# Optimization experiments

Measured on AMD Instinct MI355X. Metric: run time of the kernel, lower is better.

The kernel has to match this reference:

```python
import jax, jax.numpy as jnp
import numpy as np

MARGIN = 1.0
EPS = 1e-05
B = 8192
D = 128
NUM_CLASSES = 256


def setup_inputs() -> dict:
    key = jax.random.key(0)
    k1, k2 = jax.random.split(key)
    feature = jax.random.normal(k1, (B, D), dtype=jnp.float32)
    label = jax.random.randint(k2, (B,), 0, NUM_CLASSES, dtype=jnp.int32)
    return {"feature": feature, "label": label}


def reference(feature, label):
    # Pairwise Euclidean distance matrix: ||x_i||^2 + ||x_j||^2 - 2 x_i.x_j + eps, then sqrt
    sq = jnp.sum(feature * feature, axis=1, keepdims=True)  # [B, 1]
    dist = jnp.sqrt(jnp.maximum(sq + sq.T - 2.0 * (feature @ feature.T) + EPS, 0.0))  # [B, B]

    same = label[:, None] == label[None, :]  # [B, B] bool, includes self on diagonal
    inf = jnp.array(jnp.inf, dtype=dist.dtype)

    # Original sorts each row and takes same[1]: the SECOND smallest same-label distance
    # (the smallest is the anchor itself, distance sqrt(eps)).
    d_same = jnp.where(same, dist, inf)
    two_smallest = -jax.lax.top_k(-d_same, 2)[0]  # [B, 2], ascending smallest two
    pos = two_smallest[:, 1]  # nearest positive excluding self

    # diff.min(): hardest (closest) negative per row
    neg = jnp.min(jnp.where(same, inf, dist), axis=1)

    hinge = jnp.maximum(MARGIN + pos - neg, 0.0)
    return jnp.mean(hinge)
```

## Files before the change

kernel.cpp:

```cpp
#include <hip/hip_runtime.h>
#include <math.h>


#define BN 8192
#define MARGIN_F 1.0f
#define EPS_F 1e-5f

typedef __attribute__((ext_vector_type(8))) short short8;
typedef __attribute__((ext_vector_type(4))) float floatx4;

__device__ __forceinline__ unsigned short bf16_rne(float x, float& r) {
    unsigned u = __float_as_uint(x);
    u += 0x7FFF + ((u >> 16) & 1);
    unsigned short h = (unsigned short)(u >> 16);
    r = __uint_as_float(((unsigned)h) << 16);
    return h;
}

__global__ __launch_bounds__(256) void prep_kernel(const float* __restrict__ f,
                                                   const int* __restrict__ lbl,
                                                   short8* __restrict__ fbT,
                                                   float2* __restrict__ lsq,
                                                   float* __restrict__ g_acc,
                                                   unsigned* __restrict__ counter) {
    int gid = blockIdx.x * 256 + threadIdx.x;
    if (gid == 0) { *g_acc = 0.f; *counter = 0u; }
    int row = gid >> 3, part = gid & 7;
    const float4* f4 = (const float4*)f + (size_t)row * 32 + part * 4;
    float s = 0.f;
#pragma unroll
    for (int cc = 0; cc < 2; ++cc) {
        float4 v0 = f4[cc * 2], v1 = f4[cc * 2 + 1];
        float r0, r1, r2, r3, r4, r5, r6, r7;
        short8 o;
        o[0] = (short)bf16_rne(v0.x, r0);
        o[1] = (short)bf16_rne(v0.y, r1);
        o[2] = (short)bf16_rne(v0.z, r2);
        o[3] = (short)bf16_rne(v0.w, r3);
        o[4] = (short)bf16_rne(v1.x, r4);
        o[5] = (short)bf16_rne(v1.y, r5);
        o[6] = (short)bf16_rne(v1.z, r6);
        o[7] = (short)bf16_rne(v1.w, r7);
        fbT[(size_t)(part * 2 + cc) * BN + row] = o;
        s += r0 * r0 + r1 * r1 + r2 * r2 + r3 * r3 +
             r4 * r4 + r5 * r5 + r6 * r6 + r7 * r7;
    }
    s += __shfl_xor(s, 1, 8);
    s += __shfl_xor(s, 2, 8);
    s += __shfl_xor(s, 4, 8);
    if (part == 0) {
        float2 p;
        p.x = s;
        p.y = __int_as_float(lbl[row]);
        lsq[row] = p;
    }
}

__device__ __forceinline__ void stage_tile(const short8* __restrict__ fbT,
                                           short8* tile, int j0, int wv, int lane) {
#pragma unroll
    for (int it = 0; it < 2; ++it) {
        int s = wv * 128 + it * 64;
        int kc = (s >> 5) + (lane >> 5);
        int col = lane & 31;
        const short8* g = fbT + ((size_t)kc * BN + j0 + col);
        __builtin_amdgcn_global_load_lds(
            (const __attribute__((address_space(1))) void*)g,
            (__attribute__((address_space(3))) void*)(tile + s),
            16, 0, 0);
    }
}

__global__ __launch_bounds__(256, 2) void work_kernel(const short8* __restrict__ fbT,
                                                      const float2* __restrict__ lsq,
                                                      float* __restrict__ part_n1,
                                                      float* __restrict__ part_s1,
                                                      float* __restrict__ part_s2) {
    const int t = threadIdx.x;
    const int lane = t & 63;
    const int wv = t >> 6;
    const int q = lane >> 4, c = lane & 15;
    const int bid = blockIdx.x;

    __shared__ short8 Bt[2][512];
    __shared__ float2 lsq_sh[512];

    const int i0 = (bid & 31) * 256 + wv * 64;
    const int g = bid >> 5;
    const int jb = g * 512;

    stage_tile(fbT, Bt[0], jb, wv, lane);

    lsq_sh[t] = lsq[jb + t];
    lsq_sh[t + 256] = lsq[jb + t + 256];

    short8 a[4][4];
#pragma unroll
    for (int mf = 0; mf < 4; ++mf) {
        int row = i0 + mf * 16 + c;
#pragma unroll
        for (int ks = 0; ks < 4; ++ks)
            a[mf][ks] = fbT[(size_t)(ks * 4 + q) * BN + row];
    }
    int li[4][4];
#pragma unroll
    for (int mf = 0; mf < 4; ++mf)
#pragma unroll
        for (int rg = 0; rg < 4; ++rg)
            li[mf][rg] = __float_as_int(lsq[i0 + mf * 16 + q * 4 + rg].y);

#pragma unroll
    for (int mf = 0; mf < 4; ++mf) {
#pragma unroll
        for (int ks = 0; ks < 4; ++ks)
            asm volatile("" : "+v"(a[mf][ks]));
#pragma unroll
        for (int rg = 0; rg < 4; ++rg)
            asm volatile("" : "+v"(li[mf][rg]));
    }

    float n1[4][4], s1[4][4], s2[4][4];
#pragma unroll
    for (int mf = 0; mf < 4; ++mf)
#pragma unroll
        for (int rg = 0; rg < 4; ++rg) {
            n1[mf][rg] = INFINITY;
            s1[mf][rg] = INFINITY;
            s2[mf][rg] = INFINITY;
        }

    __syncthreads();

    for (int jt = 0; jt < 16; ++jt) {
        const short8* cur = Bt[jt & 1];
        const int j0 = jb + jt * 32;
        if (jt < 15) stage_tile(fbT, Bt[1 - (jt & 1)], j0 + 32, wv, lane);

        int ljv[2]; float sjv[2];
#pragma unroll
        for (int nf = 0; nf < 2; ++nf) {
            float2 p = lsq_sh[jt * 32 + nf * 16 + c];
            sjv[nf] = p.x;
            ljv[nf] = __float_as_int(p.y);
        }

        floatx4 acc[4][2];
#pragma unroll
        for (int mf = 0; mf < 4; ++mf)
#pragma unroll
            for (int nf = 0; nf < 2; ++nf) acc[mf][nf] = (floatx4)0.f;

#pragma unroll
        for (int ks = 0; ks < 4; ++ks) {
            short8 b[2];
#pragma unroll
            for (int nf = 0; nf < 2; ++nf)
                b[nf] = cur[(ks * 4 + q) * 32 + nf * 16 + c];
#pragma unroll
            for (int mf = 0; mf < 4; ++mf)
#pragma unroll
                for (int nf = 0; nf < 2; ++nf)
                    acc[mf][nf] = __builtin_amdgcn_mfma_f32_16x16x32_bf16(
                        a[mf][ks], b[nf], acc[mf][nf], 0, 0, 0);
        }

#pragma unroll
        for (int nf = 0; nf < 2; ++nf) {
#pragma unroll
            for (int mf = 0; mf < 4; ++mf)
#pragma unroll
                for (int rg = 0; rg < 4; ++rg) {
                    float v = fmaf(-2.0f, acc[mf][nf][rg], sjv[nf]);
                    bool same = (li[mf][rg] == ljv[nf]);
                    float vd = same ? INFINITY : v;
                    float vs = same ? v : INFINITY;
                    n1[mf][rg] = fminf(n1[mf][rg], vd);
                    s2[mf][rg] = fminf(s2[mf][rg], fmaxf(s1[mf][rg], vs));
                    s1[mf][rg] = fminf(s1[mf][rg], vs);
                }
        }
        __syncthreads();
    }

#pragma unroll
    for (int m = 1; m < 16; m <<= 1) {
#pragma unroll
        for (int mf = 0; mf < 4; ++mf)
#pragma unroll
            for (int rg = 0; rg < 4; ++rg) {
                n1[mf][rg] = fminf(n1[mf][rg], __shfl_xor(n1[mf][rg], m, 16));
                float o1 = __shfl_xor(s1[mf][rg], m, 16);
                float o2 = __shfl_xor(s2[mf][rg], m, 16);
                float hi = fminf(fmaxf(s1[mf][rg], o1), fminf(s2[mf][rg], o2));
                s1[mf][rg] = fminf(s1[mf][rg], o1);
                s2[mf][rg] = hi;
            }
    }
    if (c == 0) {
#pragma unroll
        for (int mf = 0; mf < 4; ++mf)
#pragma unroll
            for (int rg = 0; rg < 4; ++rg) {
                int idx = g * BN + i0 + mf * 16 + q * 4 + rg;
                part_n1[idx] = n1[mf][rg];
                part_s1[idx] = s1[mf][rg];
                part_s2[idx] = s2[mf][rg];
            }
    }
}

__global__ __launch_bounds__(128) void merge_kernel(const float* __restrict__ part_n1,
                                                    const float* __restrict__ part_s1,
                                                    const float* __restrict__ part_s2,
                                                    const float2* __restrict__ lsq,
                                                    float* __restrict__ g_acc,
                                                    unsigned* __restrict__ counter,
                                                    float* __restrict__ out) {
    int r = blockIdx.x * 128 + threadIdx.x;
    float n = INFINITY, s1 = INFINITY, s2 = INFINITY;
#pragma unroll
    for (int k = 0; k < 16; ++k) {
        n = fminf(n, part_n1[k * BN + r]);
        float a1 = part_s1[k * BN + r];
        float a2 = part_s2[k * BN + r];
        s2 = fminf(fmaxf(s1, a1), fminf(s2, a2));
        s1 = fminf(s1, a1);
    }
    float si = lsq[r].x;
    float pos = sqrtf(fmaxf(si + s2 + EPS_F, 0.f));
    float neg = sqrtf(fmaxf(si + n + EPS_F, 0.f));
    float h = fmaxf(MARGIN_F + pos - neg, 0.f);
    __shared__ float red[2];
#pragma unroll
    for (int m = 32; m >= 1; m >>= 1) h += __shfl_down(h, m, 64);
    if ((threadIdx.x & 63) == 0) red[threadIdx.x >> 6] = h;
    __syncthreads();
    if (threadIdx.x == 0) {
        atomicAdd(g_acc, red[0] + red[1]);
        __threadfence();
        unsigned old = atomicAdd(counter, 1u);
        if (old == 63u) {
            float tot = atomicAdd(g_acc, 0.0f);
            out[0] = tot / (float)BN;
        }
    }
}

extern "C" void kernel_launch(void* const* d_in, const int* in_sizes, int n_in,
                              void* d_out, int out_size, void* d_ws, size_t ws_size,
                              hipStream_t stream) {
    const float* f = (const float*)d_in[0];
    const int* lbl = (const int*)d_in[1];
    char* ws = (char*)d_ws;
    float2* lsq = (float2*)ws;
    short8* fbT = (short8*)(ws + 65536);
    float* part_n1 = (float*)(ws + 65536 + 2097152);
    float* part_s1 = (float*)(ws + 65536 + 2097152 + 524288);
    float* part_s2 = (float*)(ws + 65536 + 2097152 + 1048576);
    float* g_acc = (float*)(ws + 65536 + 2097152 + 1572864);
    unsigned* counter = (unsigned*)(g_acc + 1);
    float* out = (float*)d_out;

    prep_kernel<<<256, 256, 0, stream>>>(f, lbl, fbT, lsq, g_acc, counter);
    work_kernel<<<512, 256, 0, stream>>>(fbT, lsq, part_n1, part_s1, part_s2);
    merge_kernel<<<64, 128, 0, stream>>>(part_n1, part_s1, part_s2, lsq, g_acc, counter, out);
}
```

Before: 94.84 us.

## Load B fragments directly from global into registers with double buffering

Drops the LDS staging of B tiles (global_load_lds plus a per-tile __syncthreads) and has each wave load its B MFMA fragments straight from global memory into registers. A two-buffer register ping-pong prefetches the next tile while the current one is computed. This removes the LDS traffic and the block barriers, but each of the four waves now fetches the same B data from global/L2 separately, and the extra registers may cost occupancy.

```diff
diff --git a/kernel.cpp b/kernel.cpp
--- a/kernel.cpp
+++ b/kernel.cpp
@@ -56,21 +56,6 @@
     }
 }
 
-__device__ __forceinline__ void stage_tile(const short8* __restrict__ fbT,
-                                           short8* tile, int j0, int wv, int lane) {
-#pragma unroll
-    for (int it = 0; it < 2; ++it) {
-        int s = wv * 128 + it * 64;
-        int kc = (s >> 5) + (lane >> 5);
-        int col = lane & 31;
-        const short8* g = fbT + ((size_t)kc * BN + j0 + col);
-        __builtin_amdgcn_global_load_lds(
-            (const __attribute__((address_space(1))) void*)g,
-            (__attribute__((address_space(3))) void*)(tile + s),
-            16, 0, 0);
-    }
-}
-
 __global__ __launch_bounds__(256, 2) void work_kernel(const short8* __restrict__ fbT,
                                                       const float2* __restrict__ lsq,
                                                       float* __restrict__ part_n1,
@@ -82,14 +67,11 @@
     const int q = lane >> 4, c = lane & 15;
     const int bid = blockIdx.x;
 
-    __shared__ short8 Bt[2][512];
     __shared__ float2 lsq_sh[512];
 
     const int i0 = (bid & 31) * 256 + wv * 64;
     const int g = bid >> 5;
     const int jb = g * 512;
-
-    stage_tile(fbT, Bt[0], jb, wv, lane);
 
     lsq_sh[t] = lsq[jb + t];
     lsq_sh[t + 256] = lsq[jb + t + 256];
@@ -131,56 +113,56 @@
 
     __syncthreads();
 
-    for (int jt = 0; jt < 16; ++jt) {
-        const short8* cur = Bt[jt & 1];
-        const int j0 = jb + jt * 32;
-        if (jt < 15) stage_tile(fbT, Bt[1 - (jt & 1)], j0 + 32, wv, lane);
-
-        int ljv[2]; float sjv[2];
-#pragma unroll
-        for (int nf = 0; nf < 2; ++nf) {
-            float2 p = lsq_sh[jt * 32 + nf * 16 + c];
-            sjv[nf] = p.x;
-            ljv[nf] = __float_as_int(p.y);
-        }
-
-        floatx4 acc[4][2];
-#pragma unroll
-        for (int mf = 0; mf < 4; ++mf)
-#pragma unroll
-            for (int nf = 0; nf < 2; ++nf) acc[mf][nf] = (floatx4)0.f;
-
-#pragma unroll
-        for (int ks = 0; ks < 4; ++ks) {
-            short8 b[2];
-#pragma unroll
-            for (int nf = 0; nf < 2; ++nf)
-                b[nf] = cur[(ks * 4 + q) * 32 + nf * 16 + c];
-#pragma unroll
-            for (int mf = 0; mf < 4; ++mf)
-#pragma unroll
-                for (int nf = 0; nf < 2; ++nf)
-                    acc[mf][nf] = __builtin_amdgcn_mfma_f32_16x16x32_bf16(
-                        a[mf][ks], b[nf], acc[mf][nf], 0, 0, 0);
-        }
-
-#pragma unroll
-        for (int nf = 0; nf < 2; ++nf) {
-#pragma unroll
-            for (int mf = 0; mf < 4; ++mf)
-#pragma unroll
-                for (int rg = 0; rg < 4; ++rg) {
-                    float v = fmaf(-2.0f, acc[mf][nf][rg], sjv[nf]);
-                    bool same = (li[mf][rg] == ljv[nf]);
-                    float vd = same ? INFINITY : v;
-                    float vs = same ? v : INFINITY;
-                    n1[mf][rg] = fminf(n1[mf][rg], vd);
-                    s2[mf][rg] = fminf(s2[mf][rg], fmaxf(s1[mf][rg], vs));
-                    s1[mf][rg] = fminf(s1[mf][rg], vs);
-                }
-        }
-        __syncthreads();
-    }
+    const short8* bp = fbT + (size_t)q * BN + jb + c;
+
+#define LOADB(buf, jt_)                                                  \
+    do {                                                                 \
+        _Pragma("unroll") for (int ks = 0; ks < 4; ++ks)                 \
+            _Pragma("unroll") for (int nf = 0; nf < 2; ++nf)             \
+                buf[ks][nf] = bp[(size_t)ks * 4 * BN + (jt_) * 32 + nf * 16]; \
+    } while (0)
+
+#define STEP(buf, jt_)                                                   \
+    do {                                                                 \
+        int ljv[2]; float sjv[2];                                        \
+        _Pragma("unroll") for (int nf = 0; nf < 2; ++nf) {               \
+            float2 p = lsq_sh[(jt_) * 32 + nf * 16 + c];                 \
+            sjv[nf] = p.x;                                               \
+            ljv[nf] = __float_as_int(p.y);                               \
+        }                                                                \
+        floatx4 acc[4][2];                                               \
+        _Pragma("unroll") for (int mf = 0; mf < 4; ++mf)                 \
+            _Pragma("unroll") for (int nf = 0; nf < 2; ++nf)             \
+                acc[mf][nf] = (floatx4)0.f;                              \
+        _Pragma("unroll") for (int ks = 0; ks < 4; ++ks)                 \
+            _Pragma("unroll") for (int mf = 0; mf < 4; ++mf)             \
+                _Pragma("unroll") for (int nf = 0; nf < 2; ++nf)         \
+                    acc[mf][nf] = __builtin_amdgcn_mfma_f32_16x16x32_bf16( \
+                        a[mf][ks], buf[ks][nf], acc[mf][nf], 0, 0, 0);   \
+        _Pragma("unroll") for (int nf = 0; nf < 2; ++nf)                 \
+            _Pragma("unroll") for (int mf = 0; mf < 4; ++mf)             \
+                _Pragma("unroll") for (int rg = 0; rg < 4; ++rg) {       \
+                    float v = fmaf(-2.0f, acc[mf][nf][rg], sjv[nf]);     \
+                    bool same = (li[mf][rg] == ljv[nf]);                 \
+                    float vd = same ? INFINITY : v;                      \
+                    float vs = same ? v : INFINITY;                      \
+                    n1[mf][rg] = fminf(n1[mf][rg], vd);                  \
+                    s2[mf][rg] = fminf(s2[mf][rg], fmaxf(s1[mf][rg], vs)); \
+                    s1[mf][rg] = fminf(s1[mf][rg], vs);                  \
+                }                                                        \
+    } while (0)
+
+    short8 bA[4][2], bB[4][2];
+    LOADB(bA, 0);
+#pragma unroll 1
+    for (int jt = 0; jt < 16; jt += 2) {
+        LOADB(bB, jt + 1);
+        STEP(bA, jt);
+        if (jt + 2 < 16) LOADB(bA, jt + 2);
+        STEP(bB, jt + 1);
+    }
+#undef LOADB
+#undef STEP
 
 #pragma unroll
     for (int m = 1; m < 16; m <<= 1) {
```

Measured after the change: 90.74 us. -4.3%, faster.
